# Kernel tuning notes

Hardware: AMD Instinct MI355X
Metric: run time of the kernel (lower is better)

Reference implementation:

```python
import jax, jax.numpy as jnp
import numpy as np

DIM = 1024
N_HEADS = 16
HEAD_DIM = DIM // N_HEADS
D_FF = 4096
EPS = 1e-6


def setup_inputs() -> dict:
    key = jax.random.key(0)
    ks = jax.random.split(key, 8)
    B, S = 2, 2048
    s = 0.02
    return {
        "x": jax.random.normal(ks[0], (B, S, DIM), dtype=jnp.float32),
        "mask": jnp.ones((B, 1, S, S), dtype=bool),
        "wq": jax.random.normal(ks[1], (DIM, DIM), dtype=jnp.float32) * s,
        "wk": jax.random.normal(ks[2], (DIM, DIM), dtype=jnp.float32) * s,
        "wv": jax.random.normal(ks[3], (DIM, DIM), dtype=jnp.float32) * s,
        "wo": jax.random.normal(ks[4], (DIM, DIM), dtype=jnp.float32) * s,
        "w_up": jax.random.normal(ks[5], (DIM, D_FF), dtype=jnp.float32) * s,
        "b_up": jnp.zeros((D_FF,), dtype=jnp.float32),
        "w_down": jax.random.normal(ks[6], (D_FF, DIM), dtype=jnp.float32) * s,
        "b_down": jnp.zeros((DIM,), dtype=jnp.float32),
        "ln1_a": jnp.ones((DIM,), dtype=jnp.float32),
        "ln1_b": jnp.zeros((DIM,), dtype=jnp.float32),
        "ln2_a": jnp.ones((DIM,), dtype=jnp.float32),
        "ln2_b": jnp.zeros((DIM,), dtype=jnp.float32),
    }


def _layernorm(x, alpha, bias):
    mu = jnp.mean(x, axis=-1, keepdims=True)
    # torch .std() is unbiased (ddof=1); denominator is (std + eps)
    sig = jnp.std(x, axis=-1, keepdims=True, ddof=1)
    return alpha * (x - mu) / (sig + EPS) + bias


def _attention(h, wq, wk, wv, wo):
    B, S, _ = h.shape
    q = (h @ wq).reshape(B, S, N_HEADS, HEAD_DIM).transpose(0, 2, 1, 3)
    k = (h @ wk).reshape(B, S, N_HEADS, HEAD_DIM).transpose(0, 2, 1, 3)
    v = (h @ wv).reshape(B, S, N_HEADS, HEAD_DIM).transpose(0, 2, 1, 3)
    scores = jnp.einsum("bhqd,bhkd->bhqk", q, k) / jnp.sqrt(jnp.float32(HEAD_DIM))
    # NOTE: original's masked_fill result is discarded -> mask is a no-op
    probs = jax.nn.softmax(scores, axis=-1)
    out = jnp.einsum("bhqk,bhkd->bhqd", probs, v)
    out = out.transpose(0, 2, 1, 3).reshape(B, S, DIM)
    return out @ wo


def reference(x, mask, wq, wk, wv, wo, w_up, b_up, w_down, b_down,
              ln1_a, ln1_b, ln2_a, ln2_b):
    h = _layernorm(x, ln1_a, ln1_b)
    x = x + _attention(h, wq, wk, wv, wo)
    h = _layernorm(x, ln2_a, ln2_b)
    ff = (jax.nn.relu(h @ w_up + b_up)) @ w_down + b_down
    return x + ff
```

## Files before the change

kernel.cpp:

```cpp
#include <hip/hip_runtime.h>
#include <hip/hip_bf16.h>

typedef __bf16 bf16_t;
typedef __bf16 bf16x8 __attribute__((ext_vector_type(8)));
typedef __bf16 bf16x4 __attribute__((ext_vector_type(4)));
typedef float  f32x4  __attribute__((ext_vector_type(4)));

#define DIM   1024
#define NHEAD 16
#define HD    64
#define DFF   4096
#define SEQ   2048
#define NTOK  4096

__device__ __forceinline__ void lgkm_barrier() {
  asm volatile("s_waitcnt lgkmcnt(0)\n\ts_barrier" ::: "memory");
}

struct TP {
  const float *wq, *wk, *wv, *wo, *wup, *wdown;
  bf16_t *wqkvT, *wupT, *wdownT;
};

__global__ __launch_bounds__(256)
void transpose_all(TP tp) {
  __shared__ bf16_t tile[32][33];
  const int id = blockIdx.x;
  const float* src; bf16_t* dst; int M, N, bx, by;
  if (id < 4096) {
    const int w = id >> 10, t = id & 1023;
    src = (w == 0) ? tp.wq : (w == 1) ? tp.wk : (w == 2) ? tp.wv : tp.wo;
    dst = tp.wqkvT + (long)w * DIM * DIM;
    M = DIM; N = DIM; bx = (t & 31) * 32; by = (t >> 5) * 32;
  } else if (id < 8192) {
    const int t = id - 4096;
    src = tp.wup; dst = tp.wupT; M = DIM; N = DFF;
    bx = (t & 127) * 32; by = (t >> 7) * 32;
  } else {
    const int t = id - 8192;
    src = tp.wdown; dst = tp.wdownT; M = DFF; N = DIM;
    bx = (t & 31) * 32; by = (t >> 5) * 32;
  }
  const int tt = threadIdx.x;
  const int r = tt >> 3, c4 = (tt & 7) * 4;
  f32x4 v = *(const f32x4*)&src[(long)(by + r) * N + bx + c4];
  tile[r][c4 + 0] = (bf16_t)v[0]; tile[r][c4 + 1] = (bf16_t)v[1];
  tile[r][c4 + 2] = (bf16_t)v[2]; tile[r][c4 + 3] = (bf16_t)v[3];
  __syncthreads();
  bf16x4 w4;
  w4[0] = tile[c4 + 0][r]; w4[1] = tile[c4 + 1][r];
  w4[2] = tile[c4 + 2][r]; w4[3] = tile[c4 + 3][r];
  *(bf16x4*)&dst[(long)(bx + r) * M + by + c4] = w4;
}

__global__ __launch_bounds__(256)
void layernorm_k(const float* __restrict__ x, const float* __restrict__ a,
                 const float* __restrict__ b, bf16_t* __restrict__ out) {
  const int row = blockIdx.x;
  const int t   = threadIdx.x;
  const float* xr = x + (long)row * DIM;
  f32x4 v = *(const f32x4*)&xr[t * 4];
  float s1 = v[0] + v[1] + v[2] + v[3];
  float s2 = v[0]*v[0] + v[1]*v[1] + v[2]*v[2] + v[3]*v[3];
  #pragma unroll
  for (int off = 32; off > 0; off >>= 1) {
    s1 += __shfl_down(s1, off);
    s2 += __shfl_down(s2, off);
  }
  __shared__ float r1[4], r2[4];
  if ((t & 63) == 0) { r1[t >> 6] = s1; r2[t >> 6] = s2; }
  __syncthreads();
  s1 = r1[0] + r1[1] + r1[2] + r1[3];
  s2 = r2[0] + r2[1] + r2[2] + r2[3];
  const float mu = s1 * (1.0f / DIM);
  float var = (s2 - (float)DIM * mu * mu) * (1.0f / (DIM - 1));
  var = fmaxf(var, 0.0f);
  const float inv = 1.0f / (sqrtf(var) + 1e-6f);
  f32x4 av = *(const f32x4*)&a[t * 4];
  f32x4 bv = *(const f32x4*)&b[t * 4];
  bf16x4 o;
  o[0] = (bf16_t)(av[0] * (v[0] - mu) * inv + bv[0]);
  o[1] = (bf16_t)(av[1] * (v[1] - mu) * inv + bv[1]);
  o[2] = (bf16_t)(av[2] * (v[2] - mu) * inv + bv[2]);
  o[3] = (bf16_t)(av[3] * (v[3] - mu) * inv + bv[3]);
  *(bf16x4*)&out[(long)row * DIM + t * 4] = o;
}

__global__ __launch_bounds__(256)
void reduce_wo_ln(const float* __restrict__ x, const bf16_t* __restrict__ p0,
                  const bf16_t* __restrict__ p1, const float* __restrict__ a,
                  const float* __restrict__ b, bf16_t* __restrict__ x1b,
                  bf16_t* __restrict__ h2) {
  const int row = blockIdx.x;
  const int t   = threadIdx.x;
  const long base = (long)row * DIM + t * 4;
  f32x4 v = *(const f32x4*)&x[base];
  bf16x4 pa = *(const bf16x4*)&p0[base];
  bf16x4 pb = *(const bf16x4*)&p1[base];
  bf16x4 xo;
  xo[0] = (bf16_t)(v[0] + (float)pa[0] + (float)pb[0]);
  xo[1] = (bf16_t)(v[1] + (float)pa[1] + (float)pb[1]);
  xo[2] = (bf16_t)(v[2] + (float)pa[2] + (float)pb[2]);
  xo[3] = (bf16_t)(v[3] + (float)pa[3] + (float)pb[3]);
  *(bf16x4*)&x1b[base] = xo;
  const float w0 = (float)xo[0], w1 = (float)xo[1], w2 = (float)xo[2], w3 = (float)xo[3];
  float s1 = w0 + w1 + w2 + w3;
  float s2 = w0*w0 + w1*w1 + w2*w2 + w3*w3;
  #pragma unroll
  for (int off = 32; off > 0; off >>= 1) {
    s1 += __shfl_down(s1, off);
    s2 += __shfl_down(s2, off);
  }
  __shared__ float r1[4], r2[4];
  if ((t & 63) == 0) { r1[t >> 6] = s1; r2[t >> 6] = s2; }
  __syncthreads();
  s1 = r1[0] + r1[1] + r1[2] + r1[3];
  s2 = r2[0] + r2[1] + r2[2] + r2[3];
  const float mu = s1 * (1.0f / DIM);
  float var = (s2 - (float)DIM * mu * mu) * (1.0f / (DIM - 1));
  var = fmaxf(var, 0.0f);
  const float inv = 1.0f / (sqrtf(var) + 1e-6f);
  f32x4 av = *(const f32x4*)&a[t * 4];
  f32x4 bv = *(const f32x4*)&b[t * 4];
  bf16x4 o;
  o[0] = (bf16_t)(av[0] * (w0 - mu) * inv + bv[0]);
  o[1] = (bf16_t)(av[1] * (w1 - mu) * inv + bv[1]);
  o[2] = (bf16_t)(av[2] * (w2 - mu) * inv + bv[2]);
  o[3] = (bf16_t)(av[3] * (w3 - mu) * inv + bv[3]);
  *(bf16x4*)&h2[(long)row * DIM + t * 4] = o;
}

__global__ __launch_bounds__(256)
void combine_att(const bf16_t* __restrict__ O1, const float* __restrict__ l0,
                 const float* __restrict__ l1, bf16_t* __restrict__ O0_attn) {
  const long i = ((long)blockIdx.x * 256 + threadIdx.x) * 4;
  const int n = (int)(i & (DIM - 1));
  const long t = i >> 10;
  const int h = n >> 6;
  const long lidx = ((t >> 11) * NHEAD + h) * SEQ + (t & (SEQ - 1));
  const float inv = 1.0f / (l0[lidx] + l1[lidx]);
  bf16x4 a = *(const bf16x4*)&O0_attn[i];
  bf16x4 b = *(const bf16x4*)&O1[i];
  bf16x4 o;
  o[0] = (bf16_t)(((float)a[0] + (float)b[0]) * inv);
  o[1] = (bf16_t)(((float)a[1] + (float)b[1]) * inv);
  o[2] = (bf16_t)(((float)a[2] + (float)b[2]) * inv);
  o[3] = (bf16_t)(((float)a[3] + (float)b[3]) * inv);
  *(bf16x4*)&O0_attn[i] = o;
}

__global__ __launch_bounds__(256)
void reduce_fd(const bf16_t* __restrict__ x1b, const float* __restrict__ bias,
               const bf16_t* __restrict__ p0, const bf16_t* __restrict__ p1,
               float* __restrict__ out) {
  const long i = ((long)blockIdx.x * 256 + threadIdx.x) * 4;
  const int n = (int)(i & (DIM - 1));
  bf16x4 xv = *(const bf16x4*)&x1b[i];
  f32x4 bv = *(const f32x4*)&bias[n];
  bf16x4 a = *(const bf16x4*)&p0[i];
  bf16x4 b = *(const bf16x4*)&p1[i];
  f32x4 o;
  o[0] = (float)xv[0] + bv[0] + (float)a[0] + (float)b[0];
  o[1] = (float)xv[1] + bv[1] + (float)a[1] + (float)b[1];
  o[2] = (float)xv[2] + bv[2] + (float)a[2] + (float)b[2];
  o[3] = (float)xv[3] + bv[3] + (float)a[3] + (float)b[3];
  *(f32x4*)&out[i] = o;
}

enum { EPI_QKV = 1, EPI_BIAS_RELU = 3, EPI_PART = 6 };

#define BM 128
#define BK 32

template <int EPI, int TBN>
__global__ __launch_bounds__(256)
void gemm_bt(const bf16_t* __restrict__ A, int lda,
             const bf16_t* __restrict__ BT, int ldb,
             bf16_t* __restrict__ Cb, bf16_t* __restrict__ Cb2,
             const float* __restrict__ bias,
             int M, int N, int Ks) {
  __shared__ bf16_t sA[2][BM][BK];
  __shared__ bf16_t sB[2][TBN][BK];
  const int tid  = threadIdx.x;
  int lin = blockIdx.x + gridDim.x * (blockIdx.y + gridDim.y * blockIdx.z);
  const int by_ = lin % gridDim.y; lin /= gridDim.y;
  const int bx_ = lin % gridDim.x;
  const int bz_ = lin / gridDim.x;
  const int m0   = by_ * BM;
  const int n0   = bx_ * TBN;
  const long koff = (long)bz_ * Ks;
  const int lane = tid & 63, wave = tid >> 6;
  constexpr int MI = (TBN == 128) ? 4 : 2;
  const int wm = (TBN == 128) ? (wave >> 1) * 64 : wave * 32;
  const int wn = (TBN == 128) ? (wave & 1) * 64 : 0;
  const int fm = lane & 15, fq = lane >> 4;

  const int lr = lane >> 2, lc = (lane & 3) * 8;
  const bf16_t* gA0 = &A[(long)(m0 + wave * 32 + lr) * lda + koff + lc];
  const bf16_t* gA1 = gA0 + 16 * (long)lda;
  const int brow = (TBN == 128) ? wave * 32 : wave * 16;
  const bf16_t* gB0 = &BT[(long)(n0 + brow + lr) * ldb + koff + lc];
  const bf16_t* gB1 = gB0 + 16 * (long)ldb;

  f32x4 acc[MI][4] = {};
  bf16x8 rA0, rA1, rB0, rB1;

  rA0 = *(const bf16x8*)gA0;
  rA1 = *(const bf16x8*)gA1;
  rB0 = *(const bf16x8*)gB0;
  if constexpr (TBN == 128) rB1 = *(const bf16x8*)gB1;
  gA0 += BK; gA1 += BK; gB0 += BK; gB1 += BK;
  *(bf16x8*)&sA[0][wave * 32 + lr][lc]      = rA0;
  *(bf16x8*)&sA[0][wave * 32 + 16 + lr][lc] = rA1;
  *(bf16x8*)&sB[0][brow + lr][lc]           = rB0;
  if constexpr (TBN == 128) *(bf16x8*)&sB[0][wave * 32 + 16 + lr][lc] = rB1;
  if (BK < Ks) {
    rA0 = *(const bf16x8*)gA0;
    rA1 = *(const bf16x8*)gA1;
    rB0 = *(const bf16x8*)gB0;
    if constexpr (TBN == 128) rB1 = *(const bf16x8*)gB1;
    gA0 += BK; gA1 += BK; gB0 += BK; gB1 += BK;
  }
  __syncthreads();

  int p = 0;
  for (int k0 = 0; k0 < Ks; k0 += BK, p ^= 1) {
    if (k0 + BK < Ks) {
      *(bf16x8*)&sA[p ^ 1][wave * 32 + lr][lc]      = rA0;
      *(bf16x8*)&sA[p ^ 1][wave * 32 + 16 + lr][lc] = rA1;
      *(bf16x8*)&sB[p ^ 1][brow + lr][lc]           = rB0;
      if constexpr (TBN == 128) *(bf16x8*)&sB[p ^ 1][wave * 32 + 16 + lr][lc] = rB1;
      if (k0 + 2 * BK < Ks) {
        rA0 = *(const bf16x8*)gA0;
        rA1 = *(const bf16x8*)gA1;
        rB0 = *(const bf16x8*)gB0;
        if constexpr (TBN == 128) rB1 = *(const bf16x8*)gB1;
        gA0 += BK; gA1 += BK; gB0 += BK; gB1 += BK;
      }
    }
    bf16x8 af[MI], bfr[4];
    #pragma unroll
    for (int i = 0; i < MI; i++) af[i]  = *(const bf16x8*)&sA[p][wm + i * 16 + fm][fq * 8];
    #pragma unroll
    for (int j = 0; j < 4; j++)  bfr[j] = *(const bf16x8*)&sB[p][wn + j * 16 + fm][fq * 8];
    #pragma unroll
    for (int i = 0; i < MI; i++)
      #pragma unroll
      for (int j = 0; j < 4; j++)
        acc[i][j] = __builtin_amdgcn_mfma_f32_16x16x32_bf16(af[i], bfr[j], acc[i][j], 0, 0, 0);
    lgkm_barrier();
  }

  #pragma unroll
  for (int i = 0; i < MI; i++) {
    #pragma unroll
    for (int j = 0; j < 4; j++) {
      const int mb = m0 + wm + i * 16 + fq * 4;
      const int n  = n0 + wn + j * 16 + fm;
      #pragma unroll
      for (int r = 0; r < 4; r++) {
        const int m = mb + r;
        float vv = acc[i][j][r];
        if constexpr (EPI == EPI_QKV) {
          const int mat = n >> 10, h_ = (n >> 6) & 15, d_ = n & 63;
          const int b_ = m >> 11, s_ = m & 2047;
          if (mat == 2) {
            Cb2[((long)(b_ * NHEAD + h_) * HD + d_) * SEQ + s_] = (bf16_t)vv;
          } else {
            Cb[(long)mat * (32L * SEQ * HD) + (((long)(b_ * NHEAD + h_)) * SEQ + s_) * HD + d_] = (bf16_t)vv;
          }
        } else if constexpr (EPI == EPI_BIAS_RELU) {
          Cb[(long)m * N + n] = (bf16_t)fmaxf(vv + bias[n], 0.0f);
        } else {
          bf16_t* P = bz_ ? Cb2 : Cb;
          P[(long)m * N + n] = (bf16_t)vv;
        }
      }
    }
  }
}

#define KVT 128

__device__ __forceinline__ int swz(int grp, int slot) {
  return (grp * 64 + (slot ^ ((slot >> 3) & 7) ^ (grp & 1))) * 8;
}

__global__ __launch_bounds__(256)
void flash_attn(const bf16_t* __restrict__ q, const bf16_t* __restrict__ k,
                const bf16_t* __restrict__ vt,
                bf16_t* __restrict__ O0, bf16_t* __restrict__ O1,
                float* __restrict__ l0, float* __restrict__ l1) {
  __shared__ bf16_t sK[16 * 64 * 8];
  __shared__ bf16_t sV[16 * 64 * 8];

  const int tid  = threadIdx.x;
  const int bh   = blockIdx.x & 31, qb = blockIdx.x >> 5;
  const int b    = bh >> 4, h = bh & 15;
  const int lane = tid & 63, wave = tid >> 6;
  const int fm   = lane & 15, fq = lane >> 4;
  const int qw0  = qb * 128 + wave * 32;
  const int kvbase = blockIdx.y * (SEQ / 2);
  bf16_t* Op = blockIdx.y ? O1 : O0;
  float*  lp = blockIdx.y ? l1 : l0;

  const bf16_t* qh  = q  + (long)bh * SEQ * HD;
  const bf16_t* kh  = k  + (long)bh * SEQ * HD;
  const bf16_t* vth = vt + (long)bh * HD * SEQ;

  bf16x8 bQ[2][2];
  #pragma unroll
  for (int qt = 0; qt < 2; qt++)
    #pragma unroll
    for (int kk = 0; kk < 2; kk++) {
      bf16x8 v = *(const bf16x8*)&qh[(long)(qw0 + qt * 16 + fm) * HD + kk * 32 + fq * 8];
      #pragma unroll
      for (int e = 0; e < 8; e++) v[e] = (bf16_t)((float)v[e] * 0.125f);
      bQ[qt][kk] = v;
    }

  float la = 0.f, lb = 0.f;
  f32x4 oA[4] = {}, oB[4] = {};

  for (int it = 0; it < (SEQ / 2) / KVT; it++) {
    const int kv0 = kvbase + it * KVT;
    __syncthreads();
    #pragma unroll
    for (int p = 0; p < 4; p++) {
      const int id = tid + p * 256;
      {
        const int rho = id >> 3, c0 = (id & 7) * 8;
        const int u = rho >> 5, w = rho & 31;
        const int h2 = (w >> 2) & 1;
        const int fmw = ((w >> 3) << 2) | (w & 3);
        const int kk = (id >> 2) & 1, fq3 = id & 3;
        bf16x8 g = *(const bf16x8*)&kh[(long)(kv0 + rho) * HD + c0];
        *(bf16x8*)&sK[swz((u * 2 + h2) * 2 + kk, fq3 * 16 + fmw)] = g;
      }
      {
        const int d = id >> 4, c0 = (id & 15) * 8;
        const int u = c0 >> 5, fq3 = (c0 >> 3) & 3;
        const int jd = d >> 4, fmw = d & 15;
        bf16x8 g = *(const bf16x8*)&vth[(long)d * SEQ + kv0 + c0];
        *(bf16x8*)&sV[swz(u * 4 + jd, fq3 * 16 + fmw)] = g;
      }
    }
    __syncthreads();

    #pragma unroll
    for (int u = 0; u < 4; u++) {
      f32x4 stA[2], stB[2];
      #pragma unroll
      for (int h2 = 0; h2 < 2; h2++) {
        bf16x8 aK0 = *(const bf16x8*)&sK[swz((u * 2 + h2) * 2 + 0, lane)];
        bf16x8 aK1 = *(const bf16x8*)&sK[swz((u * 2 + h2) * 2 + 1, lane)];
        f32x4 z0 = {};
        z0 = __builtin_amdgcn_mfma_f32_16x16x32_bf16(aK0, bQ[0][0], z0, 0, 0, 0);
        stA[h2] = __builtin_amdgcn_mfma_f32_16x16x32_bf16(aK1, bQ[0][1], z0, 0, 0, 0);
        f32x4 z1 = {};
        z1 = __builtin_amdgcn_mfma_f32_16x16x32_bf16(aK0, bQ[1][0], z1, 0, 0, 0);
        stB[h2] = __builtin_amdgcn_mfma_f32_16x16x32_bf16(aK1, bQ[1][1], z1, 0, 0, 0);
      }
      bf16x8 pA, pB;
      #pragma unroll
      for (int h2 = 0; h2 < 2; h2++)
        #pragma unroll
        for (int r = 0; r < 4; r++) {
          const float ea = __expf(stA[h2][r]);
          const float eb = __expf(stB[h2][r]);
          la += ea; lb += eb;
          pA[h2 * 4 + r] = (bf16_t)ea;
          pB[h2 * 4 + r] = (bf16_t)eb;
        }
      #pragma unroll
      for (int jd = 0; jd < 4; jd++) {
        bf16x8 bV = *(const bf16x8*)&sV[swz(u * 4 + jd, lane)];
        oA[jd] = __builtin_amdgcn_mfma_f32_16x16x32_bf16(pA, bV, oA[jd], 0, 0, 0);
        oB[jd] = __builtin_amdgcn_mfma_f32_16x16x32_bf16(pB, bV, oB[jd], 0, 0, 0);
      }
    }
  }

  la += __shfl_xor(la, 16); la += __shfl_xor(la, 32);
  lb += __shfl_xor(lb, 16); lb += __shfl_xor(lb, 32);
  if (fq == 0) {
    lp[(long)bh * SEQ + qw0 + fm]      = la;
    lp[(long)bh * SEQ + qw0 + 16 + fm] = lb;
  }

  #pragma unroll
  for (int r = 0; r < 4; r++) {
    const long rowA = ((long)b * SEQ + qw0 + fq * 4 + r) * DIM + h * HD;
    const long rowB = rowA + 16L * DIM;
    #pragma unroll
    for (int jd = 0; jd < 4; jd++) {
      Op[rowA + jd * 16 + fm] = (bf16_t)oA[jd][r];
      Op[rowB + jd * 16 + fm] = (bf16_t)oB[jd][r];
    }
  }
}

extern "C" void kernel_launch(void* const* d_in, const int* in_sizes, int n_in,
                              void* d_out, int out_size, void* d_ws, size_t ws_size,
                              hipStream_t stream) {
  (void)in_sizes; (void)n_in; (void)out_size; (void)ws_size;
  const float* x      = (const float*)d_in[0];
  const float* wq     = (const float*)d_in[2];
  const float* wk     = (const float*)d_in[3];
  const float* wv     = (const float*)d_in[4];
  const float* wo     = (const float*)d_in[5];
  const float* w_up   = (const float*)d_in[6];
  const float* b_up   = (const float*)d_in[7];
  const float* w_down = (const float*)d_in[8];
  const float* b_down = (const float*)d_in[9];
  const float* ln1a   = (const float*)d_in[10];
  const float* ln1b   = (const float*)d_in[11];
  const float* ln2a   = (const float*)d_in[12];
  const float* ln2b   = (const float*)d_in[13];

  char* ws = (char*)d_ws;
  const size_t MB = 1ull << 20;
  const size_t KB = 1ull << 10;
  float*  l0     = (float*)(ws);
  float*  l1     = (float*)(ws + 256 * KB);
  bf16_t* wqkvT  = (bf16_t*)(ws + 512 * KB);
  bf16_t* woT    = (bf16_t*)(ws + 512 * KB + 6 * MB);
  bf16_t* h      = (bf16_t*)(ws + 9 * MB);
  bf16_t* O0     = (bf16_t*)(ws + 9 * MB);
  bf16_t* attn   = (bf16_t*)(ws + 9 * MB);
  bf16_t* qkv    = (bf16_t*)(ws + 17 * MB);
  bf16_t* qd     = (bf16_t*)(ws + 17 * MB);
  bf16_t* kd     = (bf16_t*)(ws + 25 * MB);
  bf16_t* vtd    = (bf16_t*)(ws + 33 * MB);
  bf16_t* O1     = (bf16_t*)(ws + 41 * MB);
  bf16_t* p0_wo  = (bf16_t*)(ws + 17 * MB);
  bf16_t* p1_wo  = (bf16_t*)(ws + 25 * MB);
  bf16_t* x1b    = (bf16_t*)(ws + 41 * MB);
  bf16_t* h2     = (bf16_t*)(ws);
  bf16_t* wdownT = (bf16_t*)(ws + 49 * MB);
  bf16_t* wupT   = (bf16_t*)(ws + 57 * MB);
  bf16_t* ff1    = (bf16_t*)(ws + 9 * MB);
  bf16_t* p0_fd  = (bf16_t*)(ws);
  bf16_t* p1_fd  = (bf16_t*)(ws + 57 * MB);
  float*  outp   = (float*)d_out;

  const dim3 T(256);
  TP tp{wq, wk, wv, wo, w_up, w_down, wqkvT, wupT, wdownT};
  transpose_all<<<dim3(12288), T, 0, stream>>>(tp);

  layernorm_k<<<dim3(4096), T, 0, stream>>>(x, ln1a, ln1b, h);
  gemm_bt<EPI_QKV, 128><<<dim3(24, 32), T, 0, stream>>>(h, DIM, wqkvT, DIM, qkv, vtd,
                                                        nullptr, NTOK, 3072, DIM);
  flash_attn<<<dim3(512, 2), T, 0, stream>>>(qd, kd, vtd, O0, O1, l0, l1);
  combine_att<<<dim3(NTOK * DIM / 1024), T, 0, stream>>>(O1, l0, l1, attn);
  gemm_bt<EPI_PART, 64><<<dim3(16, 32, 2), T, 0, stream>>>(attn, DIM, woT, DIM, p0_wo, p1_wo,
                                                           nullptr, NTOK, DIM, DIM / 2);
  reduce_wo_ln<<<dim3(4096), T, 0, stream>>>(x, p0_wo, p1_wo, ln2a, ln2b, x1b, h2);
  gemm_bt<EPI_BIAS_RELU, 128><<<dim3(32, 32), T, 0, stream>>>(h2, DIM, wupT, DIM, ff1, nullptr,
                                                              b_up, NTOK, DFF, DIM);
  gemm_bt<EPI_PART, 64><<<dim3(16, 32, 2), T, 0, stream>>>(ff1, DFF, wdownT, DFF, p0_fd, p1_fd,
                                                           nullptr, NTOK, DIM, DFF / 2);
  reduce_fd<<<dim3(NTOK * DIM / 1024), T, 0, stream>>>(x1b, b_down, p0_fd, p1_fd, outp);
}
```

Measured before the change: 391.7 us.

## Register-prefetch next K/V tile in flash attention and use exp2 with prescaled Q

Flash attention now issues the global loads for the next K/V tile into registers while the current tile is computed, then writes them to shared memory between two barriers. Address and swizzle offsets are computed once, outside the loop. Q is prescaled by log2(e)/sqrt(d) so softmax can use the hardware exp2 instead of __expf, and launch bounds now request 4 blocks per CU. The goal is to hide global load latency and cut exp cost, at the price of more registers that may reduce occupancy or cause spills.

```diff
diff --git a/kernel.cpp b/kernel.cpp
--- a/kernel.cpp
+++ b/kernel.cpp
@@ -286,7 +286,7 @@
   return (grp * 64 + (slot ^ ((slot >> 3) & 7) ^ (grp & 1))) * 8;
 }
 
-__global__ __launch_bounds__(256)
+__global__ __launch_bounds__(256, 4)
 void flash_attn(const bf16_t* __restrict__ q, const bf16_t* __restrict__ k,
                 const bf16_t* __restrict__ vt,
                 bf16_t* __restrict__ O0, bf16_t* __restrict__ O1,
@@ -315,38 +315,56 @@
     for (int kk = 0; kk < 2; kk++) {
       bf16x8 v = *(const bf16x8*)&qh[(long)(qw0 + qt * 16 + fm) * HD + kk * 32 + fq * 8];
       #pragma unroll
-      for (int e = 0; e < 8; e++) v[e] = (bf16_t)((float)v[e] * 0.125f);
+      for (int e = 0; e < 8; e++) v[e] = (bf16_t)((float)v[e] * 0.18033688f);
       bQ[qt][kk] = v;
     }
+
+  const bf16_t* gK[4]; const bf16_t* gV[4];
+  int oK[4], oV[4];
+  #pragma unroll
+  for (int p = 0; p < 4; p++) {
+    const int id = tid + p * 256;
+    {
+      const int rho = id >> 3, c0 = (id & 7) * 8;
+      const int u = rho >> 5, w = rho & 31;
+      const int h2 = (w >> 2) & 1;
+      const int fmw = ((w >> 3) << 2) | (w & 3);
+      const int kk = (id >> 2) & 1, fq3 = id & 3;
+      gK[p] = &kh[(long)(kvbase + rho) * HD + c0];
+      oK[p] = swz((u * 2 + h2) * 2 + kk, fq3 * 16 + fmw);
+    }
+    {
+      const int d = id >> 4, c0 = (id & 15) * 8;
+      const int u = c0 >> 5, fq3 = (c0 >> 3) & 3;
+      const int jd = d >> 4, fmw = d & 15;
+      gV[p] = &vth[(long)d * SEQ + kvbase + c0];
+      oV[p] = swz(u * 4 + jd, fq3 * 16 + fmw);
+    }
+  }
+
+  bf16x8 rK[4], rV[4];
+  #pragma unroll
+  for (int p = 0; p < 4; p++) {
+    rK[p] = *(const bf16x8*)gK[p]; gK[p] += KVT * HD;
+    rV[p] = *(const bf16x8*)gV[p]; gV[p] += KVT;
+  }
+  #pragma unroll
+  for (int p = 0; p < 4; p++) {
+    *(bf16x8*)&sK[oK[p]] = rK[p];
+    *(bf16x8*)&sV[oV[p]] = rV[p];
+  }
+  #pragma unroll
+  for (int p = 0; p < 4; p++) {
+    rK[p] = *(const bf16x8*)gK[p]; gK[p] += KVT * HD;
+    rV[p] = *(const bf16x8*)gV[p]; gV[p] += KVT;
+  }
+  __syncthreads();
 
   float la = 0.f, lb = 0.f;
   f32x4 oA[4] = {}, oB[4] = {};
-
-  for (int it = 0; it < (SEQ / 2) / KVT; it++) {
-    const int kv0 = kvbase + it * KVT;
-    __syncthreads();
-    #pragma unroll
-    for (int p = 0; p < 4; p++) {
-      const int id = tid + p * 256;
-      {
-        const int rho = id >> 3, c0 = (id & 7) * 8;
-        const int u = rho >> 5, w = rho & 31;
-        const int h2 = (w >> 2) & 1;
-        const int fmw = ((w >> 3) << 2) | (w & 3);
-        const int kk = (id >> 2) & 1, fq3 = id & 3;
-        bf16x8 g = *(const bf16x8*)&kh[(long)(kv0 + rho) * HD + c0];
-        *(bf16x8*)&sK[swz((u * 2 + h2) * 2 + kk, fq3 * 16 + fmw)] = g;
-      }
-      {
-        const int d = id >> 4, c0 = (id & 15) * 8;
-        const int u = c0 >> 5, fq3 = (c0 >> 3) & 3;
-        const int jd = d >> 4, fmw = d & 15;
-        bf16x8 g = *(const bf16x8*)&vth[(long)d * SEQ + kv0 + c0];
-        *(bf16x8*)&sV[swz(u * 4 + jd, fq3 * 16 + fmw)] = g;
-      }
-    }
-    __syncthreads();
-
+  constexpr int NIT = (SEQ / 2) / KVT;
+
+  for (int it = 0; it < NIT; it++) {
     #pragma unroll
     for (int u = 0; u < 4; u++) {
       f32x4 stA[2], stB[2];
@@ -366,8 +384,8 @@
       for (int h2 = 0; h2 < 2; h2++)
         #pragma unroll
         for (int r = 0; r < 4; r++) {
-          const float ea = __expf(stA[h2][r]);
-          const float eb = __expf(stB[h2][r]);
+          const float ea = __builtin_amdgcn_exp2f(stA[h2][r]);
+          const float eb = __builtin_amdgcn_exp2f(stB[h2][r]);
           la += ea; lb += eb;
           pA[h2 * 4 + r] = (bf16_t)ea;
           pB[h2 * 4 + r] = (bf16_t)eb;
@@ -378,6 +396,22 @@
         oA[jd] = __builtin_amdgcn_mfma_f32_16x16x32_bf16(pA, bV, oA[jd], 0, 0, 0);
         oB[jd] = __builtin_amdgcn_mfma_f32_16x16x32_bf16(pB, bV, oB[jd], 0, 0, 0);
       }
+    }
+    if (it + 1 < NIT) {
+      __syncthreads();
+      #pragma unroll
+      for (int p = 0; p < 4; p++) {
+        *(bf16x8*)&sK[oK[p]] = rK[p];
+        *(bf16x8*)&sV[oV[p]] = rV[p];
+      }
+      if (it + 2 < NIT) {
+        #pragma unroll
+        for (int p = 0; p < 4; p++) {
+          rK[p] = *(const bf16x8*)gK[p]; gK[p] += KVT * HD;
+          rV[p] = *(const bf16x8*)gV[p]; gV[p] += KVT;
+        }
+      }
+      __syncthreads();
     }
   }
 
```

Measured after the change: 489.3 us. +24.9%, slower.
